# Kernel tuning notes

Measured on AMD Instinct MI355X. Metric: run time of the kernel, lower is better.

## Reference

```python
import jax, jax.numpy as jnp
import numpy as np

B, S, D = 2, 4096, 2048
H = 16
HD = D // H          # head dim = 128
CHUNK = 64           # chunk size for O(N) chunked linear attention


def setup_inputs() -> dict:
    key = jax.random.key(0)
    ks = jax.random.split(key, 5)
    w = D ** -0.5  # fan-in init scale
    return {
        "x": jax.random.normal(ks[0], (B, S, D), jnp.float32),
        "Wq": jax.random.normal(ks[1], (D, D), jnp.float32) * w,
        "Wk": jax.random.normal(ks[2], (D, D), jnp.float32) * w,
        "Wv": jax.random.normal(ks[3], (D, D), jnp.float32) * w,
        "Wo": jax.random.normal(ks[4], (D, D), jnp.float32) * w,
    }


def _chunk_linear_attn(q, k, v):
    """Causal linear attention (identity feature map), chunked recurrent form.
    q, k, v: [b, h, n, d]. Equivalent to o_t = sum_{s<=t} (q_t . k_s) v_s.
    """
    b, h, n, d = q.shape
    nc = n // CHUNK
    q = q.reshape(b, h, nc, CHUNK, d)
    k = k.reshape(b, h, nc, CHUNK, d)
    v = v.reshape(b, h, nc, CHUNK, d)
    # intra-chunk causal part
    attn = jnp.einsum('bhncd,bhnsd->bhncs', q, k)
    causal = jnp.tril(jnp.ones((CHUNK, CHUNK), dtype=bool))
    attn = jnp.where(causal, attn, jnp.zeros((), attn.dtype))
    o_intra = jnp.einsum('bhncs,bhnsd->bhncd', attn, v)
    # inter-chunk recurrent state: S_i = sum_{j < i} K_j^T V_j  ([d, d] per head)
    kv = jnp.einsum('bhnsd,bhnse->bhnde', k, v)
    S = jnp.cumsum(kv, axis=2) - kv  # exclusive prefix sum over chunks
    o_inter = jnp.einsum('bhncd,bhnde->bhnce', q, S)
    return (o_intra + o_inter).reshape(b, h, n, d)


def reference(x, Wq, Wk, Wv, Wo):
    # bias-free projections (nn.Linear convention: y = x @ W.T)
    q = (x @ Wq.T).reshape(B, S, H, HD).transpose(0, 2, 1, 3)
    k = (x @ Wk.T).reshape(B, S, H, HD).transpose(0, 2, 1, 3)
    v = (x @ Wv.T).reshape(B, S, H, HD).transpose(0, 2, 1, 3)
    scale = HD ** -0.5  # fla chunk_linear_attn default scale on q
    o = _chunk_linear_attn(q * scale, k, v)
    o = o.transpose(0, 2, 1, 3).reshape(B, S, D)
    return o @ Wo.T
```

## Files before the change

### kernel.cpp

```cpp
#include <hip/hip_runtime.h>

typedef unsigned short u16;
typedef __attribute__((ext_vector_type(8))) short short8;
typedef __attribute__((ext_vector_type(8))) unsigned short u16x8;
typedef __attribute__((ext_vector_type(4))) unsigned short u16x4;
typedef __attribute__((ext_vector_type(2))) unsigned short u16x2;
typedef __attribute__((ext_vector_type(4))) float f32x4;

#define NBATCH 2
#define SEQ    4096
#define DIM    2048
#define NHEAD  16
#define HD     128
#define CH     64
#define NC     64
#define MROWS  8192

__device__ __forceinline__ float b2f(u16 u) {
    unsigned x = ((unsigned)u) << 16;
    return __builtin_bit_cast(float, x);
}
__device__ __forceinline__ u16 f2b(float f) {
    unsigned u = __builtin_bit_cast(unsigned, f);
    u += 0x7fffu + ((u >> 16) & 1u);
    return (u16)(u >> 16);
}

__device__ __forceinline__ void gload_lds16(const u16* g, u16* l) {
    __builtin_amdgcn_global_load_lds(
        (const __attribute__((address_space(1))) void*)g,
        (__attribute__((address_space(3))) void*)l, 16, 0, 0);
}

__global__ __launch_bounds__(256) void cast_all(
    const float* __restrict__ x,
    const float* __restrict__ w0, const float* __restrict__ w1,
    const float* __restrict__ w2, const float* __restrict__ w3,
    u16* __restrict__ xo,
    u16* __restrict__ o0, u16* __restrict__ o1,
    u16* __restrict__ o2, u16* __restrict__ o3)
{
    const int blk = blockIdx.x;
    const float* in;
    u16* out;
    long i;
    if (blk < 8192) {
        in = x; out = xo;
        i = (long)blk * 256 + threadIdx.x;
    } else {
        const int seg = (blk - 8192) >> 11;
        in  = seg == 0 ? w0 : seg == 1 ? w1 : seg == 2 ? w2 : w3;
        out = seg == 0 ? o0 : seg == 1 ? o1 : seg == 2 ? o2 : o3;
        i = (long)((blk - 8192) & 2047) * 256 + threadIdx.x;
    }
    f32x4 a = ((const f32x4*)in)[2 * i];
    f32x4 b = ((const f32x4*)in)[2 * i + 1];
    u16x8 o;
#pragma unroll
    for (int j = 0; j < 4; j++) { o[j] = f2b(a[j]); o[4 + j] = f2b(b[j]); }
    ((u16x8*)out)[i] = o;
}

#define GBM 256
#define GBN 256
#define GBK 32
#define BUFE 16384

struct Ctx8 {
    int wave, lane, wr, wc, m16, quad;
    int fl;
    long grA[2];
    int ldso[2];
};

__device__ __forceinline__ Ctx8 ctx8(int K) {
    Ctx8 c;
    const int tid = threadIdx.x;
    c.wave = tid >> 6; c.lane = tid & 63;
    c.wr = c.wave >> 2; c.wc = c.wave & 3;
    c.m16 = c.lane & 15; c.quad = (c.lane >> 4) & 3;
    const int t3 = c.lane >> 3;
    const int u3 = (c.lane & 7) ^ t3;
    const int ml = 2 * t3 + (u3 >> 2);
    const int sl = (u3 & 3) * 8;
#pragma unroll
    for (int i = 0; i < 2; i++) {
        const int bi = 2 * c.wave + i;
        c.grA[i] = (long)(bi * 16 + ml) * K + sl;
        c.ldso[i] = bi * 512 + c.lane * 8;
    }
    const int line = c.m16 >> 1;
    c.fl = line * 64 + ((((c.m16 & 1) << 2) | c.quad) ^ line) * 8;
    return c;
}

template<bool READB, bool STG, int VMC>
__device__ __forceinline__ void phase8(
    const Ctx8& c, const u16* As, const u16* Bs, const int ihalf,
    short8 (&bf)[4], f32x4 (&acc)[8][4],
    const u16* pS, long off, u16* dst)
{
    short8 af[4];
#pragma unroll
    for (int t = 0; t < 4; t++)
        af[t] = *(const short8*)&As[(c.wr * 8 + ihalf * 4 + t) * 512 + c.fl];
    if (READB) {
#pragma unroll
        for (int t = 0; t < 4; t++)
            bf[t] = *(const short8*)&Bs[(c.wc * 4 + t) * 512 + c.fl];
    }
    if (STG) {
        gload_lds16(pS + c.grA[0] + off, dst + c.ldso[0]);
        gload_lds16(pS + c.grA[1] + off, dst + c.ldso[1]);
    }
    if (VMC >= 0)
        asm volatile("s_waitcnt vmcnt(%0)" :: "i"(VMC < 0 ? 0 : VMC) : "memory");
    __builtin_amdgcn_s_barrier();
    asm volatile("s_waitcnt lgkmcnt(0)" ::: "memory");
    __builtin_amdgcn_sched_barrier(0);
    __builtin_amdgcn_s_setprio(1);
#pragma unroll
    for (int i = 0; i < 4; i++)
#pragma unroll
        for (int j = 0; j < 4; j++)
            acc[ihalf * 4 + i][j] = __builtin_amdgcn_mfma_f32_16x16x32_bf16(
                af[i], bf[j], acc[ihalf * 4 + i][j], 0, 0, 0);
    __builtin_amdgcn_s_setprio(0);
    __builtin_amdgcn_s_barrier();
}

__device__ __forceinline__ void kloop8(
    const Ctx8& c, const u16* pA, const u16* pB, int K, u16* L, f32x4 (&acc)[8][4])
{
    const int NT = K >> 5;
#pragma unroll
    for (int t = 0; t < 3; t++) {
        u16* As = L + t * BUFE;
        u16* Bs = As + 8192;
        gload_lds16(pA + c.grA[0] + t * GBK, As + c.ldso[0]);
        gload_lds16(pA + c.grA[1] + t * GBK, As + c.ldso[1]);
        gload_lds16(pB + c.grA[0] + t * GBK, Bs + c.ldso[0]);
        gload_lds16(pB + c.grA[1] + t * GBK, Bs + c.ldso[1]);
    }
    asm volatile("s_waitcnt vmcnt(8)" ::: "memory");
    __builtin_amdgcn_s_barrier();

    short8 bf[4];
#pragma unroll 1
    for (int u = 0; u < NT - 3; ++u) {
        const u16* As = L + (u & 3) * BUFE;
        const u16* Bs = As + 8192;
        u16* AsN = L + ((u + 3) & 3) * BUFE;
        const long off = (long)(u + 3) * GBK;
        phase8<true,  true, -1>(c, As, Bs, 0, bf, acc, pA, off, AsN);
        phase8<false, true,  8>(c, As, Bs, 1, bf, acc, pB, off, AsN + 8192);
    }
    {
        const u16* As = L + ((NT - 3) & 3) * BUFE;
        phase8<true,  false, -1>(c, As, As + 8192, 0, bf, acc, nullptr, 0, nullptr);
        phase8<false, false,  4>(c, As, As + 8192, 1, bf, acc, nullptr, 0, nullptr);
    }
    {
        const u16* As = L + ((NT - 2) & 3) * BUFE;
        phase8<true,  false, -1>(c, As, As + 8192, 0, bf, acc, nullptr, 0, nullptr);
        phase8<false, false,  0>(c, As, As + 8192, 1, bf, acc, nullptr, 0, nullptr);
    }
    {
        const u16* As = L + ((NT - 1) & 3) * BUFE;
        phase8<true,  false, -1>(c, As, As + 8192, 0, bf, acc, nullptr, 0, nullptr);
        phase8<false, false, -1>(c, As, As + 8192, 1, bf, acc, nullptr, 0, nullptr);
    }
}

__global__ __launch_bounds__(512, 2) void gemm_qkv(
    const u16* __restrict__ A,
    const u16* __restrict__ Wqb, const u16* __restrict__ Wkb, const u16* __restrict__ Wvb,
    u16* __restrict__ q, u16* __restrict__ k, u16* __restrict__ kt,
    u16* __restrict__ vt, float qscale)
{
    __shared__ __align__(16) u16 L[4 * BUFE];
    const Ctx8 c = ctx8(DIM);

    const int lid = blockIdx.x;
    const int swz = (lid & 7) * 96 + (lid >> 3);
    const int bx = swz & 31;
    const int by = swz >> 5;
    const int w = by >> 3;
    const long row0 = (long)bx * GBM;
    const long col0 = (long)(by & 7) * GBN;
    const u16* Bw = w == 0 ? Wqb : w == 1 ? Wkb : Wvb;

    f32x4 acc[8][4];
#pragma unroll
    for (int i = 0; i < 8; i++)
#pragma unroll
        for (int j = 0; j < 4; j++) {
            f32x4 z = {0.f, 0.f, 0.f, 0.f};
            acc[i][j] = z;
        }

    kloop8(c, A + row0 * DIM, Bw + col0 * DIM, DIM, L, acc);

    const float scale = (w == 0) ? qscale : 1.0f;
#pragma unroll
    for (int i = 0; i < 8; i++) {
        const long grow0 = row0 + c.wr * 128 + i * 16 + c.quad * 4;
#pragma unroll
        for (int j = 0; j < 4; j++) {
            const long gcol = col0 + c.wc * 64 + j * 16 + c.m16;
            u16x4 p;
#pragma unroll
            for (int r = 0; r < 4; r++) p[r] = f2b(acc[i][j][r] * scale);
            if (w == 0) {
#pragma unroll
                for (int r = 0; r < 4; r++) q[(grow0 + r) * DIM + gcol] = p[r];
            } else {
                const long b = grow0 >> 12;
                const long t0 = grow0 & (SEQ - 1);
                u16* Ct = (w == 1) ? kt : vt;
                *(u16x4*)(Ct + (b * DIM + gcol) * SEQ + t0) = p;
                if (w == 1) {
#pragma unroll
                    for (int r = 0; r < 4; r++) k[(grow0 + r) * DIM + gcol] = p[r];
                }
            }
        }
    }
}

__global__ __launch_bounds__(512, 2) void gemm_out(
    const u16* __restrict__ A, const u16* __restrict__ Bw, float* __restrict__ C)
{
    __shared__ __align__(16) u16 L[4 * BUFE];
    const Ctx8 c = ctx8(DIM);
    const int lid = blockIdx.x;
    const int swz = (lid & 7) * 32 + (lid >> 3);
    const long row0 = (long)(swz & 31) * GBM;
    const long col0 = (long)(swz >> 5) * GBN;

    f32x4 acc[8][4];
#pragma unroll
    for (int i = 0; i < 8; i++)
#pragma unroll
        for (int j = 0; j < 4; j++) {
            f32x4 z = {0.f, 0.f, 0.f, 0.f};
            acc[i][j] = z;
        }

    kloop8(c, A + row0 * DIM, Bw + col0 * DIM, DIM, L, acc);

#pragma unroll
    for (int i = 0; i < 8; i++) {
        const long grow0 = row0 + c.wr * 128 + i * 16 + c.quad * 4;
#pragma unroll
        for (int j = 0; j < 4; j++) {
            const long gcol = col0 + c.wc * 64 + j * 16 + c.m16;
#pragma unroll
            for (int r = 0; r < 4; r++)
                C[(grow0 + r) * DIM + gcol] = acc[i][j][r];
        }
    }
}

__global__ __launch_bounds__(256) void chunk_kv_mfma(
    const u16* __restrict__ Vt, const u16* __restrict__ Kt, u16* __restrict__ KV)
{
    const int tid = threadIdx.x, blk = blockIdx.x;
    const int c = blk & (NC - 1), bh = blk >> 6;
    const int wave = tid >> 6, lane = tid & 63;
    const int wr = wave >> 1, wc = wave & 1;
    const int m16 = lane & 15, quad = lane >> 4;
    const u16* vb = Vt + (long)bh * HD * SEQ + c * CH;
    const u16* kb = Kt + (long)bh * HD * SEQ + c * CH;

    f32x4 acc[4][4];
#pragma unroll
    for (int i = 0; i < 4; i++)
#pragma unroll
        for (int j = 0; j < 4; j++) {
            f32x4 z = {0.f, 0.f, 0.f, 0.f};
            acc[i][j] = z;
        }

#pragma unroll
    for (int tk = 0; tk < 2; tk++) {
        short8 af[4], bf[4];
#pragma unroll
        for (int t = 0; t < 4; t++)
            af[t] = *(const short8*)(vb + (long)(wr * 64 + t * 16 + m16) * SEQ + tk * 32 + quad * 8);
#pragma unroll
        for (int t = 0; t < 4; t++)
            bf[t] = *(const short8*)(kb + (long)(wc * 64 + t * 16 + m16) * SEQ + tk * 32 + quad * 8);
#pragma unroll
        for (int i = 0; i < 4; i++)
#pragma unroll
            for (int j = 0; j < 4; j++)
                acc[i][j] = __builtin_amdgcn_mfma_f32_16x16x32_bf16(
                    af[i], bf[j], acc[i][j], 0, 0, 0);
    }

    u16* outp = KV + (long)blk * (HD * HD);
#pragma unroll
    for (int i = 0; i < 4; i++)
#pragma unroll
        for (int j = 0; j < 4; j++)
#pragma unroll
            for (int r = 0; r < 4; r++)
                outp[(wr * 64 + i * 16 + quad * 4 + r) * HD + wc * 64 + j * 16 + m16]
                    = f2b(acc[i][j][r]);
}

__global__ __launch_bounds__(256) void kv_prefix(u16* __restrict__ KV)
{
    const int bh  = blockIdx.x >> 5;
    const int sub = blockIdx.x & 31;
    const long base = (long)bh * NC * (HD * HD) + (sub * 256 + threadIdx.x) * 2;
    float s0 = 0.f, s1 = 0.f;
#pragma unroll 4
    for (int c = 0; c < NC; c++) {
        u16* p = KV + base + (long)c * (HD * HD);
        u16x2 v = *(u16x2*)p;
        u16x2 w; w[0] = f2b(s0); w[1] = f2b(s1);
        *(u16x2*)p = w;
        s0 += b2f(v[0]); s1 += b2f(v[1]);
    }
}

#define AMP 72

__global__ __launch_bounds__(256) void chunk_out_mfma(
    const u16* __restrict__ Q, const u16* __restrict__ Kn,
    const u16* __restrict__ Vt, const u16* __restrict__ Sb, u16* __restrict__ O)
{
    __shared__ __align__(16) u16 Am[CH * AMP];

    const int tid = threadIdx.x, blk = blockIdx.x;
    const int c = blk & (NC - 1), bh = blk >> 6;
    const int h = bh & (NHEAD - 1), b = bh >> 4;
    const long rowbase = (long)b * SEQ + (long)c * CH;
    const int wave = tid >> 6, lane = tid & 63;
    const int m16 = lane & 15, quad = lane >> 4;

    const u16* qrow = Q  + (rowbase + wave * 16 + m16) * DIM + h * HD;
    const u16* krow = Kn + rowbase * DIM + h * HD;

    short8 qa[4];
#pragma unroll
    for (int dk = 0; dk < 4; dk++)
        qa[dk] = *(const short8*)(qrow + dk * 32 + quad * 8);

    f32x4 acc1[4];
#pragma unroll
    for (int jt = 0; jt < 4; jt++) {
        f32x4 z = {0.f, 0.f, 0.f, 0.f};
        acc1[jt] = z;
    }
#pragma unroll
    for (int dk = 0; dk < 4; dk++)
#pragma unroll
        for (int jt = 0; jt < 4; jt++) {
            short8 bb = *(const short8*)(krow + (long)(jt * 16 + m16) * DIM + dk * 32 + quad * 8);
            acc1[jt] = __builtin_amdgcn_mfma_f32_16x16x32_bf16(qa[dk], bb, acc1[jt], 0, 0, 0);
        }
    const int mbase = wave * 16 + quad * 4;
#pragma unroll
    for (int jt = 0; jt < 4; jt++) {
        const int j = jt * 16 + m16;
#pragma unroll
        for (int r = 0; r < 4; r++) {
            float v = (j <= mbase + r) ? acc1[jt][r] : 0.f;
            Am[(mbase + r) * AMP + j] = f2b(v);
        }
    }

    f32x4 acc[8];
#pragma unroll
    for (int et = 0; et < 8; et++) {
        f32x4 z = {0.f, 0.f, 0.f, 0.f};
        acc[et] = z;
    }
    const u16* Sg = Sb + (long)blk * (HD * HD);
#pragma unroll
    for (int dk = 0; dk < 4; dk++)
#pragma unroll
        for (int et = 0; et < 8; et++) {
            short8 sb = *(const short8*)(Sg + (et * 16 + m16) * HD + dk * 32 + quad * 8);
            acc[et] = __builtin_amdgcn_mfma_f32_16x16x32_bf16(qa[dk], sb, acc[et], 0, 0, 0);
        }

    __syncthreads();
    const u16* vb = Vt + (long)bh * HD * SEQ + c * CH;
#pragma unroll
    for (int tk = 0; tk < 2; tk++) {
        short8 a = *(const short8*)&Am[(wave * 16 + m16) * AMP + tk * 32 + quad * 8];
#pragma unroll
        for (int et = 0; et < 8; et++) {
            short8 vbf = *(const short8*)(vb + (long)(et * 16 + m16) * SEQ + tk * 32 + quad * 8);
            acc[et] = __builtin_amdgcn_mfma_f32_16x16x32_bf16(a, vbf, acc[et], 0, 0, 0);
        }
    }

#pragma unroll
    for (int et = 0; et < 8; et++) {
        const int e = et * 16 + m16;
#pragma unroll
        for (int r = 0; r < 4; r++) {
            const int m = wave * 16 + quad * 4 + r;
            O[(rowbase + m) * DIM + h * HD + e] = f2b(acc[et][r]);
        }
    }
}

extern "C" void kernel_launch(void* const* d_in, const int* in_sizes, int n_in,
                              void* d_out, int out_size, void* d_ws, size_t ws_size,
                              hipStream_t stream)
{
    (void)in_sizes; (void)n_in; (void)out_size; (void)ws_size;
    const float* x  = (const float*)d_in[0];
    const float* Wq = (const float*)d_in[1];
    const float* Wk = (const float*)d_in[2];
    const float* Wv = (const float*)d_in[3];
    const float* Wo = (const float*)d_in[4];
    float* out = (float*)d_out;

    const long NE = (long)MROWS * DIM;
    const long WE = (long)DIM * DIM;
    u16* xb  = (u16*)d_ws;
    u16* Wqb = xb  + NE;
    u16* Wkb = Wqb + WE;
    u16* Wvb = Wkb + WE;
    u16* Wob = Wvb + WE;
    u16* q   = Wob + WE;
    u16* k   = q + NE;
    u16* vt  = k + NE;
    u16* kv  = vt + NE;
    u16* o   = xb;
    u16* kt  = (u16*)d_out;

    hipLaunchKernelGGL(cast_all, dim3(16384), dim3(256), 0, stream,
                       x, Wq, Wk, Wv, Wo, xb, Wqb, Wkb, Wvb, Wob);

    const float qscale = 0.08838834764831845f;

    hipLaunchKernelGGL(gemm_qkv, dim3(768), dim3(512), 0, stream,
                       xb, Wqb, Wkb, Wvb, q, k, kt, vt, qscale);

    hipLaunchKernelGGL(chunk_kv_mfma, dim3(NBATCH * NHEAD * NC), dim3(256), 0, stream, vt, kt, kv);
    hipLaunchKernelGGL(kv_prefix,     dim3(1024),                dim3(256), 0, stream, kv);
    hipLaunchKernelGGL(chunk_out_mfma,dim3(NBATCH * NHEAD * NC), dim3(256), 0, stream, q, k, vt, kv, o);

    hipLaunchKernelGGL(gemm_out, dim3(256), dim3(512), 0, stream, o, Wob, out);
}
```

Measured before the change: 599.2 us.

## Fuse chunk KV computation with prefix sum and drop GEMM block swizzle

Merges the per-chunk K^T V kernel and the separate prefix-sum kernel into one kernel. Each block owns a 64x64 tile of one head's state and walks the 64 chunks sequentially, keeping the running sum in MFMA accumulators and writing the exclusive prefix before each update. Loads for the next chunk are double-buffered. The aim is to avoid writing and re-reading the per-chunk KV buffer and to save a launch, but only 128 blocks run a serial 64-step loop, which limits parallelism. The change also replaces the swizzled block mapping in both GEMMs with a plain 2D grid, and removes an lgkmcnt wait and sched_barrier in the MFMA phase.

```diff
diff --git a/kernel.cpp b/kernel.cpp
--- a/kernel.cpp
+++ b/kernel.cpp
@@ -116,8 +116,6 @@
     if (VMC >= 0)
         asm volatile("s_waitcnt vmcnt(%0)" :: "i"(VMC < 0 ? 0 : VMC) : "memory");
     __builtin_amdgcn_s_barrier();
-    asm volatile("s_waitcnt lgkmcnt(0)" ::: "memory");
-    __builtin_amdgcn_sched_barrier(0);
     __builtin_amdgcn_s_setprio(1);
 #pragma unroll
     for (int i = 0; i < 4; i++)
@@ -181,13 +179,9 @@
     __shared__ __align__(16) u16 L[4 * BUFE];
     const Ctx8 c = ctx8(DIM);
 
-    const int lid = blockIdx.x;
-    const int swz = (lid & 7) * 96 + (lid >> 3);
-    const int bx = swz & 31;
-    const int by = swz >> 5;
-    const int w = by >> 3;
-    const long row0 = (long)bx * GBM;
-    const long col0 = (long)(by & 7) * GBN;
+    const int w = blockIdx.y >> 3;
+    const long row0 = (long)blockIdx.x * GBM;
+    const long col0 = (long)(blockIdx.y & 7) * GBN;
     const u16* Bw = w == 0 ? Wqb : w == 1 ? Wkb : Wvb;
 
     f32x4 acc[8][4];
@@ -233,10 +227,8 @@
 {
     __shared__ __align__(16) u16 L[4 * BUFE];
     const Ctx8 c = ctx8(DIM);
-    const int lid = blockIdx.x;
-    const int swz = (lid & 7) * 32 + (lid >> 3);
-    const long row0 = (long)(swz & 31) * GBM;
-    const long col0 = (long)(swz >> 5) * GBN;
+    const long row0 = (long)blockIdx.x * GBM;
+    const long col0 = (long)blockIdx.y * GBN;
 
     f32x4 acc[8][4];
 #pragma unroll
@@ -262,68 +254,73 @@
     }
 }
 
-__global__ __launch_bounds__(256) void chunk_kv_mfma(
+__global__ __launch_bounds__(256) void chunk_kv_prefix(
     const u16* __restrict__ Vt, const u16* __restrict__ Kt, u16* __restrict__ KV)
 {
-    const int tid = threadIdx.x, blk = blockIdx.x;
-    const int c = blk & (NC - 1), bh = blk >> 6;
+    const int tid = threadIdx.x;
+    const int bh = blockIdx.x >> 2, tile = blockIdx.x & 3;
+    const int e0 = (tile >> 1) * 64, d0 = (tile & 1) * 64;
     const int wave = tid >> 6, lane = tid & 63;
     const int wr = wave >> 1, wc = wave & 1;
     const int m16 = lane & 15, quad = lane >> 4;
-    const u16* vb = Vt + (long)bh * HD * SEQ + c * CH;
-    const u16* kb = Kt + (long)bh * HD * SEQ + c * CH;
-
-    f32x4 acc[4][4];
-#pragma unroll
-    for (int i = 0; i < 4; i++)
-#pragma unroll
-        for (int j = 0; j < 4; j++) {
+
+    const u16* vb = Vt + ((long)bh * HD + e0 + wr * 32) * SEQ;
+    const u16* kb = Kt + ((long)bh * HD + d0 + wc * 32) * SEQ;
+    u16* outb = KV + (long)bh * NC * (HD * HD);
+
+    f32x4 acc[2][2];
+#pragma unroll
+    for (int i = 0; i < 2; i++)
+#pragma unroll
+        for (int j = 0; j < 2; j++) {
             f32x4 z = {0.f, 0.f, 0.f, 0.f};
             acc[i][j] = z;
         }
 
-#pragma unroll
-    for (int tk = 0; tk < 2; tk++) {
-        short8 af[4], bf[4];
-#pragma unroll
-        for (int t = 0; t < 4; t++)
-            af[t] = *(const short8*)(vb + (long)(wr * 64 + t * 16 + m16) * SEQ + tk * 32 + quad * 8);
-#pragma unroll
-        for (int t = 0; t < 4; t++)
-            bf[t] = *(const short8*)(kb + (long)(wc * 64 + t * 16 + m16) * SEQ + tk * 32 + quad * 8);
-#pragma unroll
-        for (int i = 0; i < 4; i++)
-#pragma unroll
-            for (int j = 0; j < 4; j++)
-                acc[i][j] = __builtin_amdgcn_mfma_f32_16x16x32_bf16(
-                    af[i], bf[j], acc[i][j], 0, 0, 0);
-    }
-
-    u16* outp = KV + (long)blk * (HD * HD);
-#pragma unroll
-    for (int i = 0; i < 4; i++)
-#pragma unroll
-        for (int j = 0; j < 4; j++)
-#pragma unroll
-            for (int r = 0; r < 4; r++)
-                outp[(wr * 64 + i * 16 + quad * 4 + r) * HD + wc * 64 + j * 16 + m16]
-                    = f2b(acc[i][j][r]);
-}
-
-__global__ __launch_bounds__(256) void kv_prefix(u16* __restrict__ KV)
-{
-    const int bh  = blockIdx.x >> 5;
-    const int sub = blockIdx.x & 31;
-    const long base = (long)bh * NC * (HD * HD) + (sub * 256 + threadIdx.x) * 2;
-    float s0 = 0.f, s1 = 0.f;
-#pragma unroll 4
-    for (int c = 0; c < NC; c++) {
-        u16* p = KV + base + (long)c * (HD * HD);
-        u16x2 v = *(u16x2*)p;
-        u16x2 w; w[0] = f2b(s0); w[1] = f2b(s1);
-        *(u16x2*)p = w;
-        s0 += b2f(v[0]); s1 += b2f(v[1]);
-    }
+#define KVP_LOAD(AF, BF, cc)                                                   \
+    {                                                                          \
+        const long t0 = (long)(cc) * CH + quad * 8;                            \
+        _Pragma("unroll")                                                      \
+        for (int i = 0; i < 2; i++) {                                          \
+            AF[i][0] = *(const short8*)(vb + (long)(i * 16 + m16) * SEQ + t0);      \
+            AF[i][1] = *(const short8*)(vb + (long)(i * 16 + m16) * SEQ + t0 + 32); \
+            BF[i][0] = *(const short8*)(kb + (long)(i * 16 + m16) * SEQ + t0);      \
+            BF[i][1] = *(const short8*)(kb + (long)(i * 16 + m16) * SEQ + t0 + 32); \
+        }                                                                      \
+    }
+
+#define KVP_STEP(AF, BF, cc)                                                   \
+    {                                                                          \
+        u16* op = outb + (long)(cc) * (HD * HD);                               \
+        _Pragma("unroll")                                                      \
+        for (int i = 0; i < 2; i++)                                            \
+            _Pragma("unroll")                                                  \
+            for (int j = 0; j < 2; j++)                                        \
+                _Pragma("unroll")                                              \
+                for (int r = 0; r < 4; r++)                                    \
+                    op[(long)(e0 + wr * 32 + i * 16 + quad * 4 + r) * HD       \
+                       + d0 + wc * 32 + j * 16 + m16] = f2b(acc[i][j][r]);     \
+        _Pragma("unroll")                                                      \
+        for (int tk = 0; tk < 2; tk++)                                         \
+            _Pragma("unroll")                                                  \
+            for (int i = 0; i < 2; i++)                                        \
+                _Pragma("unroll")                                              \
+                for (int j = 0; j < 2; j++)                                    \
+                    acc[i][j] = __builtin_amdgcn_mfma_f32_16x16x32_bf16(       \
+                        AF[i][tk], BF[j][tk], acc[i][j], 0, 0, 0);             \
+    }
+
+    short8 a0[2][2], b0[2][2], a1[2][2], b1[2][2];
+    KVP_LOAD(a0, b0, 0);
+#pragma unroll 1
+    for (int cc = 0; cc < NC; cc += 2) {
+        KVP_LOAD(a1, b1, cc + 1);
+        KVP_STEP(a0, b0, cc);
+        if (cc + 2 < NC) KVP_LOAD(a0, b0, cc + 2);
+        KVP_STEP(a1, b1, cc + 1);
+    }
+#undef KVP_LOAD
+#undef KVP_STEP
 }
 
 #define AMP 72
@@ -442,12 +439,11 @@
 
     const float qscale = 0.08838834764831845f;
 
-    hipLaunchKernelGGL(gemm_qkv, dim3(768), dim3(512), 0, stream,
+    hipLaunchKernelGGL(gemm_qkv, dim3(MROWS / GBM, 24), dim3(512), 0, stream,
                        xb, Wqb, Wkb, Wvb, q, k, kt, vt, qscale);
 
-    hipLaunchKernelGGL(chunk_kv_mfma, dim3(NBATCH * NHEAD * NC), dim3(256), 0, stream, vt, kt, kv);
-    hipLaunchKernelGGL(kv_prefix,     dim3(1024),                dim3(256), 0, stream, kv);
-    hipLaunchKernelGGL(chunk_out_mfma,dim3(NBATCH * NHEAD * NC), dim3(256), 0, stream, q, k, vt, kv, o);
-
-    hipLaunchKernelGGL(gemm_out, dim3(256), dim3(512), 0, stream, o, Wob, out);
-}
+    hipLaunchKernelGGL(chunk_kv_prefix, dim3(128), dim3(256), 0, stream, vt, kt, kv);
+    hipLaunchKernelGGL(chunk_out_mfma,  dim3(NBATCH * NHEAD * NC), dim3(256), 0, stream, q, k, vt, kv, o);
+
+    hipLaunchKernelGGL(gemm_out, dim3(MROWS / GBM, DIM / GBN), dim3(512), 0, stream, o, Wob, out);
+}
```

After: 587.2 us. 1.02x faster.
